# Performance work log

Measured on AMD Instinct MI355X. Metric: run time of the kernel, lower is better.

Reference implementation:

```python
import jax, jax.numpy as jnp
import numpy as np

B, Nv, Ne, Dv, De, Du = 8, 4096, 32768, 128, 128, 128
Dep, Dvp, Dup = 128, 128, 128


def setup_inputs() -> dict:
    key = jax.random.key(0)
    ks = jax.random.split(key, 11)
    s = 0.02
    return {
        "nodes": jax.random.normal(ks[0], (B, Nv, Dv), jnp.float32),
        "edges": jax.random.normal(ks[1], (B, Ne, De), jnp.float32),
        "global_u": jax.random.normal(ks[2], (B, Du), jnp.float32),
        "edge_rs": jax.random.randint(ks[3], (B, Ne, 2), 0, Nv, jnp.int32),
        "edge_masks": jax.random.randint(ks[4], (B, Ne, 1), 0, 2, jnp.int32),
        "W_edge": jax.random.normal(ks[5], (De + 2 * Dv + Du, Dep), jnp.float32) * s,
        "b_edge": jnp.zeros((Dep,), jnp.float32),
        "W_node": jax.random.normal(ks[6], (Dep + Dv + Du, Dvp), jnp.float32) * s,
        "b_node": jnp.zeros((Dvp,), jnp.float32),
        "W_glob": jax.random.normal(ks[7], (Dep + Dvp + Du, Dup), jnp.float32) * s,
        "b_glob": jnp.zeros((Dup,), jnp.float32),
    }


def reference(nodes, edges, global_u, edge_rs, edge_masks,
              W_edge, b_edge, W_node, b_node, W_glob, b_glob):
    recv = edge_rs[..., 0]  # (B,Ne)
    send = edge_rs[..., 1]
    # gather receiver / sender node features: (B,Ne,Dv)
    r_nodes = jnp.take_along_axis(nodes, jnp.broadcast_to(recv[..., None], (B, Ne, Dv)), axis=1)
    s_nodes = jnp.take_along_axis(nodes, jnp.broadcast_to(send[..., None], (B, Ne, Dv)), axis=1)
    u_e = jnp.broadcast_to(global_u[:, None, :], (B, Ne, Du))

    # edge block: MLP on concat -> (B,Ne,Dep)
    edge_in = jnp.concatenate([edges, r_nodes, s_nodes, u_e], -1)
    edges_p = jax.nn.relu(edge_in @ W_edge + b_edge)

    # e2v merge: masked segment-sum of edges onto receiver nodes -> (B,Nv,Dep)
    mask = edge_masks.astype(edges_p.dtype)  # (B,Ne,1)
    e2v = jax.vmap(lambda e, r: jax.ops.segment_sum(e, r, num_segments=Nv))(edges_p * mask, recv)

    # node block
    u_n = jnp.broadcast_to(global_u[:, None, :], (B, Nv, Du))
    node_in = jnp.concatenate([e2v, nodes, u_n], -1)
    nodes_p = jax.nn.relu(node_in @ W_node + b_node)

    # global block: sum-pool edges and nodes
    e2u = edges_p.sum(axis=1)  # (B,Dep)
    v2u = nodes_p.sum(axis=1)  # (B,Dvp)
    global_in = jnp.concatenate([e2u, v2u, global_u], -1)
    global_u_p = jax.nn.relu(global_in @ W_glob + b_glob)

    return (nodes_p, edges_p, global_u_p)
```

## Files before the change

kernel.cpp:

```cpp
#include <hip/hip_runtime.h>
#include <hip/hip_bf16.h>

#define B  8
#define NV 4096
#define NE 32768
#define D  128
#define KE2 384
#define KN2 256
#define KG 384

using short8    = __attribute__((ext_vector_type(8))) short;
using f32x4     = __attribute__((ext_vector_type(4))) float;
using ushort4_t = __attribute__((ext_vector_type(4))) unsigned short;

__device__ inline unsigned short f2bf(float f) {
    unsigned u = __builtin_bit_cast(unsigned, f);
    u += 0x7FFFu + ((u >> 16) & 1u);
    return (unsigned short)(u >> 16);
}
__device__ inline float bf2f(unsigned short h) {
    unsigned u = ((unsigned)h) << 16;
    return __builtin_bit_cast(float, u);
}
__device__ inline short8 cvt8(float4 a, float4 b) {
    union { __hip_bfloat162 h[4]; short8 v; } u;
    u.h[0] = __float22bfloat162_rn(make_float2(a.x, a.y));
    u.h[1] = __float22bfloat162_rn(make_float2(a.z, a.w));
    u.h[2] = __float22bfloat162_rn(make_float2(b.x, b.y));
    u.h[3] = __float22bfloat162_rn(make_float2(b.z, b.w));
    return u.v;
}

__global__ __launch_bounds__(256) void prep_weights(
    const float* __restrict__ We, const float* __restrict__ Wn,
    unsigned short* __restrict__ WtE1, unsigned short* __restrict__ WtP,
    unsigned short* __restrict__ WtN1)
{
    const int idx   = blockIdx.x * 256 + threadIdx.x;
    const int which = idx >> 14;
    const int r     = idx & 16383;
    const int n     = r >> 7, k = r & 127;
    if (which == 0)      WtE1[r]             = f2bf(We[(size_t)k * D + n]);
    else if (which == 1) WtP[r]              = f2bf(We[(size_t)(128 + k) * D + n]);
    else if (which == 2) WtP[16384 + r]      = f2bf(We[(size_t)(256 + k) * D + n]);
    else if (which == 3) WtP[2 * 16384 + r]  = f2bf(Wn[(size_t)(128 + k) * D + n]);
    else                 WtN1[r]             = f2bf(Wn[(size_t)k * D + n]);
}

__global__ __launch_bounds__(128) void bias_kernel(
    const float* __restrict__ gu,
    const float* __restrict__ We, const float* __restrict__ be,
    const float* __restrict__ Wn, const float* __restrict__ bn,
    float* __restrict__ bias_e, float* __restrict__ bias_n)
{
    const int b = blockIdx.x, n = threadIdx.x;
    float se = be[n], sn = bn[n];
    for (int k = 0; k < D; ++k) {
        const float uk = gu[(size_t)b * D + k];
        se += uk * We[(size_t)(KE2 + k) * D + n];
        sn += uk * Wn[(size_t)(KN2 + k) * D + n];
    }
    bias_e[(size_t)b * D + n] = se;
    bias_n[(size_t)b * D + n] = sn;
}

__global__ __launch_bounds__(256) void hist_kernel(
    const int* __restrict__ edge_rs, const int* __restrict__ edge_masks,
    int* __restrict__ cnt)
{
    const int idx = blockIdx.x * 256 + threadIdx.x;
    if (edge_masks[idx]) {
        const int b = idx >> 15;
        const int r = edge_rs[2 * idx];
        atomicAdd(cnt + b * NV + r, 1);
    }
}

__global__ __launch_bounds__(1024) void scan_kernel(
    const int* __restrict__ cnt, int* __restrict__ off, int* __restrict__ cur)
{
    const int b = blockIdx.x, t = threadIdx.x;
    __shared__ int part[1024];
    int4 c = *(const int4*)(cnt + b * NV + t * 4);
    const int s0 = c.x, s1 = s0 + c.y, s2 = s1 + c.z, s3 = s2 + c.w;
    part[t] = s3;
    __syncthreads();
    #pragma unroll
    for (int d = 1; d < 1024; d <<= 1) {
        const int v = (t >= d) ? part[t - d] : 0;
        __syncthreads();
        part[t] += v;
        __syncthreads();
    }
    const int base = part[t] - s3;
    int* o = off + b * (NV + 1) + t * 4;
    o[0] = base; o[1] = base + s0; o[2] = base + s1; o[3] = base + s2;
    int4 cc = { base, base + s0, base + s1, base + s2 };
    *(int4*)(cur + b * NV + t * 4) = cc;
    if (t == 1023) off[b * (NV + 1) + NV] = part[1023];
}

__global__ __launch_bounds__(256) void scatter_kernel(
    const int* __restrict__ edge_rs, const int* __restrict__ edge_masks,
    int* __restrict__ cur, int* __restrict__ elist)
{
    const int idx = blockIdx.x * 256 + threadIdx.x;
    if (edge_masks[idx]) {
        const int b = idx >> 15;
        const int e = idx & (NE - 1);
        const int r = edge_rs[2 * idx];
        const int pos = atomicAdd(cur + b * NV + r, 1);
        elist[b * NE + pos] = e;
    }
}

__global__ __launch_bounds__(512, 4) void gemm_nodes_kernel(
    const float* __restrict__ nodes,
    const unsigned short* __restrict__ WtP,
    unsigned short* __restrict__ Yp)
{
    __shared__ unsigned short Ash[128 * 128];
    __shared__ unsigned short Wsh[128 * 128];

    const int tid  = threadIdx.x;
    const int bid  = blockIdx.x;
    const int b    = bid & 7;
    const int rest = bid >> 3;
    const int tile = rest & 31;
    const int part = rest >> 5;
    const int n0   = tile * 128;

    const int srow = tid >> 2;
    const int sq   = tid & 3;
    const int sX   = (srow & 7) << 3;

    {
        const float* src = nodes + ((size_t)b * NV + n0 + srow) * D + sq * 32;
        #pragma unroll
        for (int j = 0; j < 4; ++j) {
            const float4 a = *(const float4*)(src + j * 8);
            const float4 c = *(const float4*)(src + j * 8 + 4);
            *(short8*)(Ash + srow * 128 + ((sq * 32 + j * 8) ^ sX)) = cvt8(a, c);
        }
        const unsigned short* ws = WtP + (size_t)part * 16384 + srow * 128 + sq * 32;
        #pragma unroll
        for (int j = 0; j < 4; ++j)
            *(short8*)(Wsh + srow * 128 + ((sq * 32 + j * 8) ^ sX)) = *(const short8*)(ws + j * 8);
    }
    __syncthreads();

    const int lane = tid & 63;
    const int wv   = tid >> 6;
    const int wr   = wv >> 2, wc = wv & 3;
    const int lc   = lane & 15, lg = lane >> 4;

    f32x4 acc[4][2] = {};
    #pragma unroll
    for (int ksub = 0; ksub < 4; ++ksub) {
        const int k = ksub * 32 + lg * 8;
        short8 afr[4], bfr[2];
        #pragma unroll
        for (int mt = 0; mt < 4; ++mt) {
            const int row = wr * 64 + mt * 16 + lc;
            afr[mt] = *(const short8*)(Ash + row * 128 + (k ^ ((row & 7) << 3)));
        }
        #pragma unroll
        for (int nt = 0; nt < 2; ++nt) {
            const int row = wc * 32 + nt * 16 + lc;
            bfr[nt] = *(const short8*)(Wsh + row * 128 + (k ^ ((row & 7) << 3)));
        }
        #pragma unroll
        for (int mt = 0; mt < 4; ++mt)
            #pragma unroll
            for (int nt = 0; nt < 2; ++nt)
                acc[mt][nt] = __builtin_amdgcn_mfma_f32_16x16x32_bf16(
                                  bfr[nt], afr[mt], acc[mt][nt], 0, 0, 0);
    }

    #pragma unroll
    for (int nt = 0; nt < 2; ++nt) {
        const int f0 = wc * 32 + nt * 16 + lg * 4;
        #pragma unroll
        for (int mt = 0; mt < 4; ++mt) {
            const int row = wr * 64 + mt * 16 + lc;
            ushort4_t p = { f2bf(acc[mt][nt][0]), f2bf(acc[mt][nt][1]),
                            f2bf(acc[mt][nt][2]), f2bf(acc[mt][nt][3]) };
            *(ushort4_t*)(Yp + ((size_t)b * NV + n0 + row) * 384 + part * 128 + f0) = p;
        }
    }
}

__global__ __launch_bounds__(512, 4) void edge_kernel(
    const float* __restrict__ edges,
    const int*   __restrict__ edge_rs,
    const unsigned short* __restrict__ WtE1,
    const unsigned short* __restrict__ Yp,
    const float* __restrict__ bias_e,
    float* __restrict__ edges_p,
    float* __restrict__ pe)
{
    __shared__ unsigned short Ash[128 * 128];
    __shared__ unsigned short Wsh[128 * 128];

    const int tid  = threadIdx.x;
    const int bid  = blockIdx.x;
    const int b    = bid & 7;
    const int tile = bid >> 3;
    const int e0   = tile * 128;

    const int srow = tid >> 2;
    const int sq   = tid & 3;
    const int sX   = (srow & 7) << 3;

    const int2 rs = ((const int2*)edge_rs)[(size_t)b * NE + e0 + srow];

    {
        const float* src = edges + ((size_t)b * NE + e0 + srow) * D + sq * 32;
        #pragma unroll
        for (int j = 0; j < 4; ++j) {
            const float4 a = *(const float4*)(src + j * 8);
            const float4 c = *(const float4*)(src + j * 8 + 4);
            *(short8*)(Ash + srow * 128 + ((sq * 32 + j * 8) ^ sX)) = cvt8(a, c);
        }
        const unsigned short* ws = WtE1 + srow * 128 + sq * 32;
        #pragma unroll
        for (int j = 0; j < 4; ++j)
            *(short8*)(Wsh + srow * 128 + ((sq * 32 + j * 8) ^ sX)) = *(const short8*)(ws + j * 8);
    }
    __syncthreads();

    const int lane = tid & 63;
    const int wv   = tid >> 6;
    const int wr   = wv >> 2, wc = wv & 3;
    const int lc   = lane & 15, lg = lane >> 4;

    f32x4 acc[4][2] = {};
    #pragma unroll
    for (int ksub = 0; ksub < 4; ++ksub) {
        const int k = ksub * 32 + lg * 8;
        short8 afr[4], bfr[2];
        #pragma unroll
        for (int mt = 0; mt < 4; ++mt) {
            const int row = wr * 64 + mt * 16 + lc;
            afr[mt] = *(const short8*)(Ash + row * 128 + (k ^ ((row & 7) << 3)));
        }
        #pragma unroll
        for (int nt = 0; nt < 2; ++nt) {
            const int row = wc * 32 + nt * 16 + lc;
            bfr[nt] = *(const short8*)(Wsh + row * 128 + (k ^ ((row & 7) << 3)));
        }
        #pragma unroll
        for (int mt = 0; mt < 4; ++mt)
            #pragma unroll
            for (int nt = 0; nt < 2; ++nt)
                acc[mt][nt] = __builtin_amdgcn_mfma_f32_16x16x32_bf16(
                                  bfr[nt], afr[mt], acc[mt][nt], 0, 0, 0);
    }
    __syncthreads();

    {
        const unsigned short* y2 = Yp + ((size_t)b * NV + rs.x) * 384 +       sq * 32;
        const unsigned short* y3 = Yp + ((size_t)b * NV + rs.y) * 384 + 128 + sq * 32;
        #pragma unroll
        for (int j = 0; j < 4; ++j) {
            *(short8*)(Ash + srow * 128 + ((sq * 32 + j * 8) ^ sX)) = *(const short8*)(y2 + j * 8);
            *(short8*)(Wsh + srow * 128 + ((sq * 32 + j * 8) ^ sX)) = *(const short8*)(y3 + j * 8);
        }
    }
    __syncthreads();

    #pragma unroll
    for (int nt = 0; nt < 2; ++nt) {
        const int f0 = wc * 32 + nt * 16 + lg * 4;
        const float4 bb = *(const float4*)(bias_e + (size_t)b * D + f0);
        float4 ps = make_float4(0.f, 0.f, 0.f, 0.f);
        #pragma unroll
        for (int mt = 0; mt < 4; ++mt) {
            const int row = wr * 64 + mt * 16 + lc;
            const int sw  = (row & 7) << 3;
            const ushort4_t y2v = *(const ushort4_t*)(Ash + row * 128 + (f0 ^ sw));
            const ushort4_t y3v = *(const ushort4_t*)(Wsh + row * 128 + (f0 ^ sw));
            float4 o;
            o.x = fmaxf(acc[mt][nt][0] + bf2f(y2v.x) + bf2f(y3v.x) + bb.x, 0.f);
            o.y = fmaxf(acc[mt][nt][1] + bf2f(y2v.y) + bf2f(y3v.y) + bb.y, 0.f);
            o.z = fmaxf(acc[mt][nt][2] + bf2f(y2v.z) + bf2f(y3v.z) + bb.z, 0.f);
            o.w = fmaxf(acc[mt][nt][3] + bf2f(y2v.w) + bf2f(y3v.w) + bb.w, 0.f);
            *(float4*)(edges_p + ((size_t)b * NE + e0 + row) * D + f0) = o;
            ps.x += o.x; ps.y += o.y; ps.z += o.z; ps.w += o.w;
        }
        #pragma unroll
        for (int m = 1; m < 16; m <<= 1) {
            ps.x += __shfl_xor(ps.x, m);
            ps.y += __shfl_xor(ps.y, m);
            ps.z += __shfl_xor(ps.z, m);
            ps.w += __shfl_xor(ps.w, m);
        }
        if (lc == 0)
            *(float4*)(pe + (((size_t)b * 256 + tile) * 2 + wr) * D + f0) = ps;
    }
}

__global__ __launch_bounds__(256, 3) void node_kernel(
    const float* __restrict__ edges_p,
    const int*   __restrict__ off,
    const int*   __restrict__ elist,
    const unsigned short* __restrict__ WtN1,
    const unsigned short* __restrict__ Yp,
    const float* __restrict__ bias_n,
    float* __restrict__ nodes_p,
    float* __restrict__ pn)
{
    __shared__ unsigned short Ash[64 * 128];
    __shared__ unsigned short Wsh[128 * 128];

    const int tid  = threadIdx.x;
    const int bid  = blockIdx.x;
    const int b    = bid & 7;
    const int tile = bid >> 3;
    const int n0   = tile * 64;

    const int srow = tid >> 2;
    const int sq   = tid & 3;
    const int sX   = (srow & 7) << 3;
    const int srw  = tid >> 1;
    const int sh   = tid & 1;
    const int sXW  = (srw & 7) << 3;

    {
        const int vtx = n0 + srow;
        const int p0  = off[b * (NV + 1) + vtx];
        const int p1  = off[b * (NV + 1) + vtx + 1];
        float4 s[8] = {};
        for (int p = p0; p < p1; ++p) {
            const int e = elist[b * NE + p];
            const float* src = edges_p + ((size_t)b * NE + e) * D + sq * 32;
            #pragma unroll
            for (int j = 0; j < 8; ++j) {
                const float4 x = *(const float4*)(src + j * 4);
                s[j].x += x.x; s[j].y += x.y; s[j].z += x.z; s[j].w += x.w;
            }
        }
        #pragma unroll
        for (int j = 0; j < 4; ++j)
            *(short8*)(Ash + srow * 128 + ((sq * 32 + j * 8) ^ sX)) =
                cvt8(s[2 * j], s[2 * j + 1]);

        const unsigned short* ws = WtN1 + srw * 128 + sh * 64;
        #pragma unroll
        for (int j = 0; j < 8; ++j)
            *(short8*)(Wsh + srw * 128 + ((sh * 64 + j * 8) ^ sXW)) = *(const short8*)(ws + j * 8);
    }
    __syncthreads();

    const int lane = tid & 63;
    const int wv   = tid >> 6;
    const int wr   = wv >> 1, wc = wv & 1;
    const int lc   = lane & 15, lg = lane >> 4;

    f32x4 acc[2][4] = {};
    #pragma unroll
    for (int ksub = 0; ksub < 4; ++ksub) {
        const int k = ksub * 32 + lg * 8;
        short8 afr[2], bfr[4];
        #pragma unroll
        for (int mt = 0; mt < 2; ++mt) {
            const int row = wr * 32 + mt * 16 + lc;
            afr[mt] = *(const short8*)(Ash + row * 128 + (k ^ ((row & 7) << 3)));
        }
        #pragma unroll
        for (int nt = 0; nt < 4; ++nt) {
            const int row = wc * 64 + nt * 16 + lc;
            bfr[nt] = *(const short8*)(Wsh + row * 128 + (k ^ ((row & 7) << 3)));
        }
        #pragma unroll
        for (int mt = 0; mt < 2; ++mt)
            #pragma unroll
            for (int nt = 0; nt < 4; ++nt)
                acc[mt][nt] = __builtin_amdgcn_mfma_f32_16x16x32_bf16(
                                  bfr[nt], afr[mt], acc[mt][nt], 0, 0, 0);
    }

    #pragma unroll
    for (int nt = 0; nt < 4; ++nt) {
        const int f0 = wc * 64 + nt * 16 + lg * 4;
        const float4 bb = *(const float4*)(bias_n + (size_t)b * D + f0);
        float4 ps = make_float4(0.f, 0.f, 0.f, 0.f);
        #pragma unroll
        for (int mt = 0; mt < 2; ++mt) {
            const int row = wr * 32 + mt * 16 + lc;
            const int v   = n0 + row;
            const ushort4_t y4v = *(const ushort4_t*)(Yp + ((size_t)b * NV + v) * 384 + 256 + f0);
            float4 o;
            o.x = fmaxf(acc[mt][nt][0] + bf2f(y4v.x) + bb.x, 0.f);
            o.y = fmaxf(acc[mt][nt][1] + bf2f(y4v.y) + bb.y, 0.f);
            o.z = fmaxf(acc[mt][nt][2] + bf2f(y4v.z) + bb.z, 0.f);
            o.w = fmaxf(acc[mt][nt][3] + bf2f(y4v.w) + bb.w, 0.f);
            *(float4*)(nodes_p + ((size_t)b * NV + v) * D + f0) = o;
            ps.x += o.x; ps.y += o.y; ps.z += o.z; ps.w += o.w;
        }
        #pragma unroll
        for (int m = 1; m < 16; m <<= 1) {
            ps.x += __shfl_xor(ps.x, m);
            ps.y += __shfl_xor(ps.y, m);
            ps.z += __shfl_xor(ps.z, m);
            ps.w += __shfl_xor(ps.w, m);
        }
        if (lc == 0)
            *(float4*)(pn + (((size_t)b * 64 + tile) * 2 + wr) * D + f0) = ps;
    }
}

__global__ __launch_bounds__(256) void reduce_kernel(
    const float* __restrict__ pe, const float* __restrict__ pn,
    float* __restrict__ e2u, float* __restrict__ v2u)
{
    __shared__ float redE[2][128], redN[2][128];
    const int b = blockIdx.x;
    const int j = threadIdx.x & 127;
    const int h = threadIdx.x >> 7;
    float s = 0.f;
    for (int i = h * 256; i < h * 256 + 256; ++i)
        s += pe[((size_t)b * 512 + i) * D + j];
    float t = 0.f;
    for (int i = h * 64; i < h * 64 + 64; ++i)
        t += pn[((size_t)b * 128 + i) * D + j];
    redE[h][j] = s;
    redN[h][j] = t;
    __syncthreads();
    if (h == 0) {
        e2u[(size_t)b * D + j] = redE[0][j] + redE[1][j];
        v2u[(size_t)b * D + j] = redN[0][j] + redN[1][j];
    }
}

__global__ __launch_bounds__(128) void glob_kernel(
    const float* __restrict__ e2u,
    const float* __restrict__ v2u,
    const float* __restrict__ gu,
    const float* __restrict__ W_glob,
    const float* __restrict__ b_glob,
    float* __restrict__ glob_p)
{
    __shared__ float gin[KG];
    const int b = blockIdx.x;
    const int j = threadIdx.x;

    gin[j      ] = e2u[(size_t)b * D + j];
    gin[j + 128] = v2u[(size_t)b * D + j];
    gin[j + 256] = gu [(size_t)b * D + j];
    __syncthreads();

    float acc = b_glob[j];
    #pragma unroll 4
    for (int k = 0; k < KG; ++k)
        acc += gin[k] * W_glob[(size_t)k * D + j];
    glob_p[(size_t)b * D + j] = fmaxf(acc, 0.f);
}

extern "C" void kernel_launch(void* const* d_in, const int* in_sizes, int n_in,
                              void* d_out, int out_size, void* d_ws, size_t ws_size,
                              hipStream_t stream) {
    const float* nodes      = (const float*)d_in[0];
    const float* edges      = (const float*)d_in[1];
    const float* gu         = (const float*)d_in[2];
    const int*   edge_rs    = (const int*)d_in[3];
    const int*   edge_masks = (const int*)d_in[4];
    const float* W_edge     = (const float*)d_in[5];
    const float* b_edge     = (const float*)d_in[6];
    const float* W_node     = (const float*)d_in[7];
    const float* b_node     = (const float*)d_in[8];
    const float* W_glob     = (const float*)d_in[9];
    const float* b_glob     = (const float*)d_in[10];

    float* out     = (float*)d_out;
    float* nodes_p = out;
    float* edges_p = out + (size_t)B * NV * D;
    float* glob_p  = edges_p + (size_t)B * NE * D;

    int*   cnt    = (int*)d_ws;
    int*   off    = cnt + (size_t)B * NV;
    int*   cur    = off + (size_t)B * (NV + 1);
    int*   elist  = cur + (size_t)B * NV;
    float* e2u    = (float*)(elist + (size_t)B * NE);
    float* v2u    = e2u + (size_t)B * D;
    float* bias_e = v2u + (size_t)B * D;
    float* bias_n = bias_e + (size_t)B * D;
    float* pe     = bias_n + (size_t)B * D;
    float* pn     = pe + (size_t)B * 512 * D;
    unsigned short* Yp   = (unsigned short*)(pn + (size_t)B * 128 * D);
    unsigned short* WtE1 = Yp + (size_t)B * NV * 384;
    unsigned short* WtP  = WtE1 + 16384;
    unsigned short* WtN1 = WtP + 3 * 16384;

    hipMemsetAsync(cnt, 0, (size_t)B * NV * sizeof(int), stream);

    prep_weights<<<(5 * 16384) / 256, 256, 0, stream>>>(W_edge, W_node, WtE1, WtP, WtN1);
    bias_kernel<<<B, 128, 0, stream>>>(gu, W_edge, b_edge, W_node, b_node, bias_e, bias_n);
    hist_kernel<<<(B * NE) / 256, 256, 0, stream>>>(edge_rs, edge_masks, cnt);
    scan_kernel<<<B, 1024, 0, stream>>>(cnt, off, cur);
    scatter_kernel<<<(B * NE) / 256, 256, 0, stream>>>(edge_rs, edge_masks, cur, elist);

    gemm_nodes_kernel<<<3 * 32 * B, 512, 0, stream>>>(nodes, WtP, Yp);
    edge_kernel<<<(NE / 128) * B, 512, 0, stream>>>(edges, edge_rs, WtE1, Yp,
                                                    bias_e, edges_p, pe);
    node_kernel<<<(NV / 64) * B, 256, 0, stream>>>(edges_p, off, elist, WtN1, Yp,
                                                   bias_n, nodes_p, pn);
    reduce_kernel<<<B, 256, 0, stream>>>(pe, pn, e2u, v2u);
    glob_kernel<<<B, 128, 0, stream>>>(e2u, v2u, gu, W_glob, b_glob, glob_p);
}
```

Measured before the change: 205.8 us.

## Halve edge tile to 64 rows and gather node projections directly in epilogue

The edge kernel now processes 64 edges per block instead of 128, doubling the grid and cutting LDS use. The receiver/sender projected-node rows are read straight from global memory in the epilogue, using indices staged in shared memory, which removes the second LDS staging pass and two barriers. The partial-sum buffer and reduce kernel are resized to match. In exchange, each block reloads the 32 KB weight tile, giving twice as many weight loads overall, and the epilogue's gathered global reads are narrow and uncoalesced.

```diff
diff --git a/kernel.cpp b/kernel.cpp
--- a/kernel.cpp
+++ b/kernel.cpp
@@ -199,33 +199,41 @@
     float* __restrict__ edges_p,
     float* __restrict__ pe)
 {
-    __shared__ unsigned short Ash[128 * 128];
+    __shared__ unsigned short Ash[64 * 128];
     __shared__ unsigned short Wsh[128 * 128];
+    __shared__ int rsl[2][64];
 
     const int tid  = threadIdx.x;
     const int bid  = blockIdx.x;
     const int b    = bid & 7;
     const int tile = bid >> 3;
-    const int e0   = tile * 128;
-
-    const int srow = tid >> 2;
-    const int sq   = tid & 3;
+    const int e0   = tile * 64;
+
+    const int srow = tid >> 3;
+    const int sq   = tid & 7;
     const int sX   = (srow & 7) << 3;
-
-    const int2 rs = ((const int2*)edge_rs)[(size_t)b * NE + e0 + srow];
-
+    const int srw  = tid >> 2;
+    const int sh   = tid & 3;
+    const int sXW  = (srw & 7) << 3;
+
+    if (tid < 64) {
+        const int2 rs = ((const int2*)edge_rs)[(size_t)b * NE + e0 + tid];
+        rsl[0][tid] = rs.x;
+        rsl[1][tid] = rs.y;
+    }
     {
-        const float* src = edges + ((size_t)b * NE + e0 + srow) * D + sq * 32;
-        #pragma unroll
-        for (int j = 0; j < 4; ++j) {
-            const float4 a = *(const float4*)(src + j * 8);
-            const float4 c = *(const float4*)(src + j * 8 + 4);
-            *(short8*)(Ash + srow * 128 + ((sq * 32 + j * 8) ^ sX)) = cvt8(a, c);
-        }
-        const unsigned short* ws = WtE1 + srow * 128 + sq * 32;
+        const float* src = edges + ((size_t)b * NE + e0 + srow) * D + sq * 16;
+        const float4 a0 = *(const float4*)(src);
+        const float4 a1 = *(const float4*)(src + 4);
+        const float4 a2 = *(const float4*)(src + 8);
+        const float4 a3 = *(const float4*)(src + 12);
+        *(short8*)(Ash + srow * 128 + ((sq * 16    ) ^ sX)) = cvt8(a0, a1);
+        *(short8*)(Ash + srow * 128 + ((sq * 16 + 8) ^ sX)) = cvt8(a2, a3);
+
+        const unsigned short* ws = WtE1 + srw * 128 + sh * 32;
         #pragma unroll
         for (int j = 0; j < 4; ++j)
-            *(short8*)(Wsh + srow * 128 + ((sq * 32 + j * 8) ^ sX)) = *(const short8*)(ws + j * 8);
+            *(short8*)(Wsh + srw * 128 + ((sh * 32 + j * 8) ^ sXW)) = *(const short8*)(ws + j * 8);
     }
     __syncthreads();
 
@@ -234,14 +242,14 @@
     const int wr   = wv >> 2, wc = wv & 3;
     const int lc   = lane & 15, lg = lane >> 4;
 
-    f32x4 acc[4][2] = {};
+    f32x4 acc[2][2] = {};
     #pragma unroll
     for (int ksub = 0; ksub < 4; ++ksub) {
         const int k = ksub * 32 + lg * 8;
-        short8 afr[4], bfr[2];
-        #pragma unroll
-        for (int mt = 0; mt < 4; ++mt) {
-            const int row = wr * 64 + mt * 16 + lc;
+        short8 afr[2], bfr[2];
+        #pragma unroll
+        for (int mt = 0; mt < 2; ++mt) {
+            const int row = wr * 32 + mt * 16 + lc;
             afr[mt] = *(const short8*)(Ash + row * 128 + (k ^ ((row & 7) << 3)));
         }
         #pragma unroll
@@ -250,24 +258,12 @@
             bfr[nt] = *(const short8*)(Wsh + row * 128 + (k ^ ((row & 7) << 3)));
         }
         #pragma unroll
-        for (int mt = 0; mt < 4; ++mt)
+        for (int mt = 0; mt < 2; ++mt)
             #pragma unroll
             for (int nt = 0; nt < 2; ++nt)
                 acc[mt][nt] = __builtin_amdgcn_mfma_f32_16x16x32_bf16(
                                   bfr[nt], afr[mt], acc[mt][nt], 0, 0, 0);
     }
-    __syncthreads();
-
-    {
-        const unsigned short* y2 = Yp + ((size_t)b * NV + rs.x) * 384 +       sq * 32;
-        const unsigned short* y3 = Yp + ((size_t)b * NV + rs.y) * 384 + 128 + sq * 32;
-        #pragma unroll
-        for (int j = 0; j < 4; ++j) {
-            *(short8*)(Ash + srow * 128 + ((sq * 32 + j * 8) ^ sX)) = *(const short8*)(y2 + j * 8);
-            *(short8*)(Wsh + srow * 128 + ((sq * 32 + j * 8) ^ sX)) = *(const short8*)(y3 + j * 8);
-        }
-    }
-    __syncthreads();
 
     #pragma unroll
     for (int nt = 0; nt < 2; ++nt) {
@@ -275,11 +271,11 @@
         const float4 bb = *(const float4*)(bias_e + (size_t)b * D + f0);
         float4 ps = make_float4(0.f, 0.f, 0.f, 0.f);
         #pragma unroll
-        for (int mt = 0; mt < 4; ++mt) {
-            const int row = wr * 64 + mt * 16 + lc;
-            const int sw  = (row & 7) << 3;
-            const ushort4_t y2v = *(const ushort4_t*)(Ash + row * 128 + (f0 ^ sw));
-            const ushort4_t y3v = *(const ushort4_t*)(Wsh + row * 128 + (f0 ^ sw));
+        for (int mt = 0; mt < 2; ++mt) {
+            const int row = wr * 32 + mt * 16 + lc;
+            const int rv  = rsl[0][row], sv = rsl[1][row];
+            const ushort4_t y2v = *(const ushort4_t*)(Yp + ((size_t)b * NV + rv) * 384 + f0);
+            const ushort4_t y3v = *(const ushort4_t*)(Yp + ((size_t)b * NV + sv) * 384 + 128 + f0);
             float4 o;
             o.x = fmaxf(acc[mt][nt][0] + bf2f(y2v.x) + bf2f(y3v.x) + bb.x, 0.f);
             o.y = fmaxf(acc[mt][nt][1] + bf2f(y2v.y) + bf2f(y3v.y) + bb.y, 0.f);
@@ -296,7 +292,7 @@
             ps.w += __shfl_xor(ps.w, m);
         }
         if (lc == 0)
-            *(float4*)(pe + (((size_t)b * 256 + tile) * 2 + wr) * D + f0) = ps;
+            *(float4*)(pe + (((size_t)b * 512 + tile) * 2 + wr) * D + f0) = ps;
     }
 }
 
@@ -419,8 +415,8 @@
     const int j = threadIdx.x & 127;
     const int h = threadIdx.x >> 7;
     float s = 0.f;
-    for (int i = h * 256; i < h * 256 + 256; ++i)
-        s += pe[((size_t)b * 512 + i) * D + j];
+    for (int i = h * 512; i < h * 512 + 512; ++i)
+        s += pe[((size_t)b * 1024 + i) * D + j];
     float t = 0.f;
     for (int i = h * 64; i < h * 64 + 64; ++i)
         t += pn[((size_t)b * 128 + i) * D + j];
@@ -486,7 +482,7 @@
     float* bias_e = v2u + (size_t)B * D;
     float* bias_n = bias_e + (size_t)B * D;
     float* pe     = bias_n + (size_t)B * D;
-    float* pn     = pe + (size_t)B * 512 * D;
+    float* pn     = pe + (size_t)B * 1024 * D;
     unsigned short* Yp   = (unsigned short*)(pn + (size_t)B * 128 * D);
     unsigned short* WtE1 = Yp + (size_t)B * NV * 384;
     unsigned short* WtP  = WtE1 + 16384;
@@ -501,8 +497,8 @@
     scatter_kernel<<<(B * NE) / 256, 256, 0, stream>>>(edge_rs, edge_masks, cur, elist);
 
     gemm_nodes_kernel<<<3 * 32 * B, 512, 0, stream>>>(nodes, WtP, Yp);
-    edge_kernel<<<(NE / 128) * B, 512, 0, stream>>>(edges, edge_rs, WtE1, Yp,
-                                                    bias_e, edges_p, pe);
+    edge_kernel<<<(NE / 64) * B, 512, 0, stream>>>(edges, edge_rs, WtE1, Yp,
+                                                   bias_e, edges_p, pe);
     node_kernel<<<(NV / 64) * B, 256, 0, stream>>>(edges_p, off, elist, WtN1, Yp,
                                                    bias_n, nodes_p, pn);
     reduce_kernel<<<B, 256, 0, stream>>>(pe, pn, e2u, v2u);
```

Measured after the change: 239.9 us. 1.17x slower.

## Fuse node-feature projection into node kernel with double-buffered K=256 GEMM

Applied to the files above, without the earlier changes.

The node half of the node-block weight is no longer projected in gemm_nodes_kernel and stored as bf16 in Yp. The node kernel now computes the full K=256 GEMM over [e2v, nodes] itself, using 128-node tiles of 512 threads and a double-buffered LDS pipeline over four 64-wide K chunks. This removes one third of the precompute GEMM and its Yp round trip, and keeps the nodes term in fp32 until conversion. The cost is more MFMA work and more global loads of node rows inside the node kernel, which now has half as many blocks.

```diff
diff --git a/kernel.cpp b/kernel.cpp
--- a/kernel.cpp
+++ b/kernel.cpp
@@ -34,17 +34,23 @@
 __global__ __launch_bounds__(256) void prep_weights(
     const float* __restrict__ We, const float* __restrict__ Wn,
     unsigned short* __restrict__ WtE1, unsigned short* __restrict__ WtP,
-    unsigned short* __restrict__ WtN1)
-{
-    const int idx   = blockIdx.x * 256 + threadIdx.x;
-    const int which = idx >> 14;
-    const int r     = idx & 16383;
-    const int n     = r >> 7, k = r & 127;
-    if (which == 0)      WtE1[r]             = f2bf(We[(size_t)k * D + n]);
-    else if (which == 1) WtP[r]              = f2bf(We[(size_t)(128 + k) * D + n]);
-    else if (which == 2) WtP[16384 + r]      = f2bf(We[(size_t)(256 + k) * D + n]);
-    else if (which == 3) WtP[2 * 16384 + r]  = f2bf(Wn[(size_t)(128 + k) * D + n]);
-    else                 WtN1[r]             = f2bf(Wn[(size_t)k * D + n]);
+    unsigned short* __restrict__ WtN)
+{
+    const int idx = blockIdx.x * 256 + threadIdx.x;
+    if (idx < 16384) {
+        const int n = idx >> 7, k = idx & 127;
+        WtE1[idx] = f2bf(We[(size_t)k * D + n]);
+    } else if (idx < 16384 + 32768) {
+        const int r  = idx - 16384;
+        const int p  = r >> 14;
+        const int rr = r & 16383;
+        const int n  = rr >> 7, k = rr & 127;
+        WtP[r] = f2bf(We[(size_t)(128 + p * 128 + k) * D + n]);
+    } else {
+        const int r = idx - 16384 - 32768;
+        const int n = r >> 8, k = r & 255;
+        WtN[r] = f2bf(Wn[(size_t)k * D + n]);
+    }
 }
 
 __global__ __launch_bounds__(128) void bias_kernel(
@@ -185,7 +191,7 @@
             const int row = wr * 64 + mt * 16 + lc;
             ushort4_t p = { f2bf(acc[mt][nt][0]), f2bf(acc[mt][nt][1]),
                             f2bf(acc[mt][nt][2]), f2bf(acc[mt][nt][3]) };
-            *(ushort4_t*)(Yp + ((size_t)b * NV + n0 + row) * 384 + part * 128 + f0) = p;
+            *(ushort4_t*)(Yp + ((size_t)b * NV + n0 + row) * 256 + part * 128 + f0) = p;
         }
     }
 }
@@ -259,8 +265,8 @@
     __syncthreads();
 
     {
-        const unsigned short* y2 = Yp + ((size_t)b * NV + rs.x) * 384 +       sq * 32;
-        const unsigned short* y3 = Yp + ((size_t)b * NV + rs.y) * 384 + 128 + sq * 32;
+        const unsigned short* y2 = Yp + ((size_t)b * NV + rs.x) * 256 +       sq * 32;
+        const unsigned short* y3 = Yp + ((size_t)b * NV + rs.y) * 256 + 128 + sq * 32;
         #pragma unroll
         for (int j = 0; j < 4; ++j) {
             *(short8*)(Ash + srow * 128 + ((sq * 32 + j * 8) ^ sX)) = *(const short8*)(y2 + j * 8);
@@ -300,137 +306,148 @@
     }
 }
 
-__global__ __launch_bounds__(256, 3) void node_kernel(
+__global__ __launch_bounds__(512, 4) void node_kernel(
+    const float* __restrict__ nodes,
     const float* __restrict__ edges_p,
     const int*   __restrict__ off,
     const int*   __restrict__ elist,
-    const unsigned short* __restrict__ WtN1,
-    const unsigned short* __restrict__ Yp,
+    const unsigned short* __restrict__ WtN,
     const float* __restrict__ bias_n,
     float* __restrict__ nodes_p,
     float* __restrict__ pn)
 {
-    __shared__ unsigned short Ash[64 * 128];
-    __shared__ unsigned short Wsh[128 * 128];
+    __shared__ unsigned short Albuf[2][128 * 64];
+    __shared__ unsigned short Wlbuf[2][128 * 64];
 
     const int tid  = threadIdx.x;
     const int bid  = blockIdx.x;
     const int b    = bid & 7;
     const int tile = bid >> 3;
-    const int n0   = tile * 64;
+    const int n0   = tile * 128;
 
     const int srow = tid >> 2;
     const int sq   = tid & 3;
     const int sX   = (srow & 7) << 3;
-    const int srw  = tid >> 1;
-    const int sh   = tid & 1;
-    const int sXW  = (srw & 7) << 3;
-
-    {
-        const int vtx = n0 + srow;
-        const int p0  = off[b * (NV + 1) + vtx];
-        const int p1  = off[b * (NV + 1) + vtx + 1];
-        float4 s[8] = {};
-        for (int p = p0; p < p1; ++p) {
-            const int e = elist[b * NE + p];
-            const float* src = edges_p + ((size_t)b * NE + e) * D + sq * 32;
-            #pragma unroll
-            for (int j = 0; j < 8; ++j) {
-                const float4 x = *(const float4*)(src + j * 4);
-                s[j].x += x.x; s[j].y += x.y; s[j].z += x.z; s[j].w += x.w;
-            }
-        }
-        #pragma unroll
-        for (int j = 0; j < 4; ++j)
-            *(short8*)(Ash + srow * 128 + ((sq * 32 + j * 8) ^ sX)) =
-                cvt8(s[2 * j], s[2 * j + 1]);
-
-        const unsigned short* ws = WtN1 + srw * 128 + sh * 64;
-        #pragma unroll
-        for (int j = 0; j < 8; ++j)
-            *(short8*)(Wsh + srw * 128 + ((sh * 64 + j * 8) ^ sXW)) = *(const short8*)(ws + j * 8);
-    }
-    __syncthreads();
+
+    const int vtx = n0 + srow;
+    const int p0  = off[b * (NV + 1) + vtx];
+    const int p1  = off[b * (NV + 1) + vtx + 1];
+    const float* nsrc = nodes + ((size_t)b * NV + vtx) * D;
 
     const int lane = tid & 63;
     const int wv   = tid >> 6;
-    const int wr   = wv >> 1, wc = wv & 1;
+    const int wr   = wv >> 2, wc = wv & 3;
     const int lc   = lane & 15, lg = lane >> 4;
-
-    f32x4 acc[2][4] = {};
-    #pragma unroll
-    for (int ksub = 0; ksub < 4; ++ksub) {
-        const int k = ksub * 32 + lg * 8;
-        short8 afr[2], bfr[4];
-        #pragma unroll
-        for (int mt = 0; mt < 2; ++mt) {
-            const int row = wr * 32 + mt * 16 + lc;
-            afr[mt] = *(const short8*)(Ash + row * 128 + (k ^ ((row & 7) << 3)));
-        }
-        #pragma unroll
-        for (int nt = 0; nt < 4; ++nt) {
-            const int row = wc * 64 + nt * 16 + lc;
-            bfr[nt] = *(const short8*)(Wsh + row * 128 + (k ^ ((row & 7) << 3)));
-        }
-        #pragma unroll
-        for (int mt = 0; mt < 2; ++mt)
+    const int lX   = (lc & 7) << 3;
+
+    float4 av[2], av2[2];
+    short8 wstg[2];
+
+    auto loadA = [&](int t) {
+        if (t < 2) {
+            float4 s0 = {}, s1 = {}, s2 = {}, s3 = {};
+            const int koff = (t & 1) * 64 + sq * 16;
+            for (int p = p0; p < p1; ++p) {
+                const int e = elist[b * NE + p];
+                const float* src = edges_p + ((size_t)b * NE + e) * D + koff;
+                const float4 x0 = *(const float4*)(src);
+                const float4 x1 = *(const float4*)(src + 4);
+                const float4 x2 = *(const float4*)(src + 8);
+                const float4 x3 = *(const float4*)(src + 12);
+                s0.x += x0.x; s0.y += x0.y; s0.z += x0.z; s0.w += x0.w;
+                s1.x += x1.x; s1.y += x1.y; s1.z += x1.z; s1.w += x1.w;
+                s2.x += x2.x; s2.y += x2.y; s2.z += x2.z; s2.w += x2.w;
+                s3.x += x3.x; s3.y += x3.y; s3.z += x3.z; s3.w += x3.w;
+            }
+            av[0] = s0; av[1] = s1; av2[0] = s2; av2[1] = s3;
+        } else {
+            const float* src = nsrc + (t - 2) * 64 + sq * 16;
+            av[0]  = *(const float4*)(src);
+            av[1]  = *(const float4*)(src + 4);
+            av2[0] = *(const float4*)(src + 8);
+            av2[1] = *(const float4*)(src + 12);
+        }
+    };
+    auto loadW = [&](int t) {
+        const unsigned short* src = WtN + (size_t)srow * KN2 + t * 64 + sq * 16;
+        wstg[0] = *(const short8*)(src);
+        wstg[1] = *(const short8*)(src + 8);
+    };
+    auto writeStage = [&](int buf) {
+        unsigned short* Al = Albuf[buf];
+        unsigned short* Wl = Wlbuf[buf];
+        const int g0 = sq * 16;
+        *(short8*)(Al + srow * 64 + ((g0    ) ^ sX)) = cvt8(av[0], av[1]);
+        *(short8*)(Al + srow * 64 + ((g0 + 8) ^ sX)) = cvt8(av2[0], av2[1]);
+        *(short8*)(Wl + srow * 64 + ((g0    ) ^ sX)) = wstg[0];
+        *(short8*)(Wl + srow * 64 + ((g0 + 8) ^ sX)) = wstg[1];
+    };
+
+    f32x4 acc[4][2] = {};
+    auto compute = [&](int buf) {
+        const unsigned short* Al = Albuf[buf];
+        const unsigned short* Wl = Wlbuf[buf];
+        #pragma unroll
+        for (int ksub = 0; ksub < 2; ++ksub) {
+            const int k = ksub * 32 + lg * 8;
+            short8 afr[4], bfr[2];
             #pragma unroll
-            for (int nt = 0; nt < 4; ++nt)
-                acc[mt][nt] = __builtin_amdgcn_mfma_f32_16x16x32_bf16(
-                                  bfr[nt], afr[mt], acc[mt][nt], 0, 0, 0);
-    }
-
-    #pragma unroll
-    for (int nt = 0; nt < 4; ++nt) {
-        const int f0 = wc * 64 + nt * 16 + lg * 4;
-        const float4 bb = *(const float4*)(bias_n + (size_t)b * D + f0);
-        float4 ps = make_float4(0.f, 0.f, 0.f, 0.f);
-        #pragma unroll
-        for (int mt = 0; mt < 2; ++mt) {
-            const int row = wr * 32 + mt * 16 + lc;
-            const int v   = n0 + row;
-            const ushort4_t y4v = *(const ushort4_t*)(Yp + ((size_t)b * NV + v) * 384 + 256 + f0);
-            float4 o;
-            o.x = fmaxf(acc[mt][nt][0] + bf2f(y4v.x) + bb.x, 0.f);
-            o.y = fmaxf(acc[mt][nt][1] + bf2f(y4v.y) + bb.y, 0.f);
-            o.z = fmaxf(acc[mt][nt][2] + bf2f(y4v.z) + bb.z, 0.f);
-            o.w = fmaxf(acc[mt][nt][3] + bf2f(y4v.w) + bb.w, 0.f);
-            *(float4*)(nodes_p + ((size_t)b * NV + v) * D + f0) = o;
-            ps.x += o.x; ps.y += o.y; ps.z += o.z; ps.w += o.w;
-        }
-        #pragma unroll
-        for (int m = 1; m < 16; m <<= 1) {
-            ps.x += __shfl_xor(ps.x, m);
-            ps.y += __shfl_xor(ps.y, m);
-            ps.z += __shfl_xor(ps.z, m);
-            ps.w += __shfl_xor(ps.w, m);
-        }
-        if (lc == 0)
-            *(float4*)(pn + (((size_t)b * 64 + tile) * 2 + wr) * D + f0) = ps;
-    }
-}
-
-__global__ __launch_bounds__(256) void reduce_kernel(
+            for (int mt = 0; mt < 4; ++mt)
+                afr[mt] = *(const short8*)(Al + (wr * 64 + mt * 16 + lc) * 64 + (k ^ lX));
+            #pragma unroll
+            for (int nt = 0; nt < 2; ++nt)
+                bfr[nt] = *(const short8*)(Wl + (wc * 32 + nt * 16 + lc) * 64 + (k ^ lX));
+            #pragma unroll
+            for (int mt = 0; mt < 4; ++mt)
+                #pragma unroll
+                for (int nt = 0; nt < 2; ++nt)
+                    acc[mt][nt] = __builtin_amdgcn_mfma_f32_16x16x32_bf16(
+                                      afr[mt], bfr[nt], acc[mt][nt], 0, 0, 0);
+        }
+    };
+
+    loadA(0); loadW(0); writeStage(0);
+    __syncthreads();
+    #pragma unroll
+    for (int t = 0; t < 4; ++t) {
+        if (t < 3) { loadA(t + 1); loadW(t + 1); }
+        compute(t & 1);
+        if (t < 3) writeStage((t + 1) & 1);
+        __syncthreads();
+    }
+
+    #pragma unroll
+    for (int nt = 0; nt < 2; ++nt) {
+        const int col = wc * 32 + nt * 16 + lc;
+        const float bias = bias_n[(size_t)b * D + col];
+        float csum = 0.f;
+        #pragma unroll
+        for (int mt = 0; mt < 4; ++mt)
+            #pragma unroll
+            for (int r = 0; r < 4; ++r) {
+                const int row = wr * 64 + mt * 16 + lg * 4 + r;
+                const float v = fmaxf(acc[mt][nt][r] + bias, 0.f);
+                nodes_p[((size_t)b * NV + n0 + row) * D + col] = v;
+                csum += v;
+            }
+        csum += __shfl_xor(csum, 16);
+        csum += __shfl_xor(csum, 32);
+        if (lg == 0)
+            pn[(((size_t)b * 32 + tile) * 2 + wr) * D + col] = csum;
+    }
+}
+
+__global__ __launch_bounds__(128) void reduce_kernel(
     const float* __restrict__ pe, const float* __restrict__ pn,
     float* __restrict__ e2u, float* __restrict__ v2u)
 {
-    __shared__ float redE[2][128], redN[2][128];
-    const int b = blockIdx.x;
-    const int j = threadIdx.x & 127;
-    const int h = threadIdx.x >> 7;
+    const int b = blockIdx.x, j = threadIdx.x;
     float s = 0.f;
-    for (int i = h * 256; i < h * 256 + 256; ++i)
-        s += pe[((size_t)b * 512 + i) * D + j];
+    for (int i = 0; i < 512; ++i) s += pe[((size_t)b * 512 + i) * D + j];
+    e2u[(size_t)b * D + j] = s;
     float t = 0.f;
-    for (int i = h * 64; i < h * 64 + 64; ++i)
-        t += pn[((size_t)b * 128 + i) * D + j];
-    redE[h][j] = s;
-    redN[h][j] = t;
-    __syncthreads();
-    if (h == 0) {
-        e2u[(size_t)b * D + j] = redE[0][j] + redE[1][j];
-        v2u[(size_t)b * D + j] = redN[0][j] + redN[1][j];
-    }
+    for (int i = 0; i < 64; ++i) t += pn[((size_t)b * 64 + i) * D + j];
+    v2u[(size_t)b * D + j] = t;
 }
 
 __global__ __launch_bounds__(128) void glob_kernel(
@@ -487,24 +504,24 @@
     float* bias_n = bias_e + (size_t)B * D;
     float* pe     = bias_n + (size_t)B * D;
     float* pn     = pe + (size_t)B * 512 * D;
-    unsigned short* Yp   = (unsigned short*)(pn + (size_t)B * 128 * D);
-    unsigned short* WtE1 = Yp + (size_t)B * NV * 384;
+    unsigned short* Yp   = (unsigned short*)(pn + (size_t)B * 64 * D);
+    unsigned short* WtE1 = Yp + (size_t)B * NV * 256;
     unsigned short* WtP  = WtE1 + 16384;
-    unsigned short* WtN1 = WtP + 3 * 16384;
+    unsigned short* WtN  = WtP + 2 * 16384;
 
     hipMemsetAsync(cnt, 0, (size_t)B * NV * sizeof(int), stream);
 
-    prep_weights<<<(5 * 16384) / 256, 256, 0, stream>>>(W_edge, W_node, WtE1, WtP, WtN1);
+    prep_weights<<<(81920 + 255) / 256, 256, 0, stream>>>(W_edge, W_node, WtE1, WtP, WtN);
     bias_kernel<<<B, 128, 0, stream>>>(gu, W_edge, b_edge, W_node, b_node, bias_e, bias_n);
     hist_kernel<<<(B * NE) / 256, 256, 0, stream>>>(edge_rs, edge_masks, cnt);
     scan_kernel<<<B, 1024, 0, stream>>>(cnt, off, cur);
     scatter_kernel<<<(B * NE) / 256, 256, 0, stream>>>(edge_rs, edge_masks, cur, elist);
 
-    gemm_nodes_kernel<<<3 * 32 * B, 512, 0, stream>>>(nodes, WtP, Yp);
+    gemm_nodes_kernel<<<2 * 32 * B, 512, 0, stream>>>(nodes, WtP, Yp);
     edge_kernel<<<(NE / 128) * B, 512, 0, stream>>>(edges, edge_rs, WtE1, Yp,
                                                     bias_e, edges_p, pe);
-    node_kernel<<<(NV / 64) * B, 256, 0, stream>>>(edges_p, off, elist, WtN1, Yp,
-                                                   bias_n, nodes_p, pn);
-    reduce_kernel<<<B, 256, 0, stream>>>(pe, pn, e2u, v2u);
+    node_kernel<<<(NV / 128) * B, 512, 0, stream>>>(nodes, edges_p, off, elist,
+                                                    WtN, bias_n, nodes_p, pn);
+    reduce_kernel<<<B, 128, 0, stream>>>(pe, pn, e2u, v2u);
     glob_kernel<<<B, 128, 0, stream>>>(e2u, v2u, gu, W_glob, b_glob, glob_p);
 }
```

After: 199.8 us. 2.9% less time.
